# Performance work log

Hardware: AMD Instinct MI355X
Metric: run time of the kernel (lower is better)

The kernel has to match this reference:

```python
import jax, jax.numpy as jnp
import numpy as np

B, KEY, D, U, MODES = 16384, 64, 128, 128, 32

def setup_inputs() -> dict:
    key = jax.random.key(0)
    k1, k2, k3, k4, k5 = jax.random.split(key, 5)
    return {
        "key": jax.random.normal(k1, (B, KEY), dtype=jnp.float32),
        "x": jax.random.normal(k2, (B, D), dtype=jnp.float32),
        "sens": jnp.ones((MODES,), dtype=jnp.float32),
        "keys_map": jax.random.normal(k3, (MODES, KEY), dtype=jnp.float32),
        "kernels": jax.random.normal(k4, (MODES, D, U), dtype=jnp.float32) * 0.05,
        "biases": jax.random.normal(k5, (MODES, U), dtype=jnp.float32) * 0.05,
    }

def reference(key, x, sens, keys_map, kernels, biases):
    # key: [B, KEY]; keys_map: [MODES, KEY]
    # Euclidean distance of each key to each mode's stored key.
    dist = jnp.sqrt(jnp.sum((key[:, None, :] - keys_map[None, :, :]) ** 2, axis=-1))  # [B, MODES]
    sim = jax.nn.softmax(sens / (dist + 1.0), axis=-1)  # [B, MODES]
    modes = kernels.shape[0]
    # Original: kernel_b = mean_m(sim[b,m] * kernels[m]); out_b = x_b @ kernel_b.
    # Reordered as GEMM-per-mode + weighted combine (same math):
    out = jnp.einsum('bm,bd,mdu->bu', sim, x, kernels) / modes  # [B, U]
    out = out + (sim @ biases) / modes  # mean over modes of sim-weighted biases
    return out
```

## Files before the change

kernel.cpp:

```cpp
#include <hip/hip_runtime.h>

#define BATCH 16384
#define KEYD  64
#define DDIM  128
#define UDIM  128
#define MODES 32

typedef __attribute__((ext_vector_type(8))) short bf16x8;
typedef __attribute__((ext_vector_type(4))) float f32x4;

__device__ __forceinline__ unsigned short f2bf(float f) {
  unsigned u = __float_as_uint(f);
  unsigned r = (u + 0x7FFFu + ((u >> 16) & 1u)) >> 16;
  return (unsigned short)r;
}

__device__ __forceinline__ void gld_lds16(const void* g, void* l) {
  __builtin_amdgcn_global_load_lds(
      (const __attribute__((address_space(1))) unsigned int*)g,
      (__attribute__((address_space(3))) unsigned int*)l, 16, 0, 0);
}

__global__ __launch_bounds__(256) void prep_all(
    const float* __restrict__ key, const float* __restrict__ x,
    const float* __restrict__ sens, const float* __restrict__ keys_map,
    const float* __restrict__ kernels, const float* __restrict__ biases,
    float* __restrict__ sim, unsigned short* __restrict__ x16,
    unsigned short* __restrict__ kb16, unsigned short* __restrict__ bb16) {
  const int t = threadIdx.x;
  const int bid = blockIdx.x;

  if (bid < BATCH / 32) {
    __shared__ float kr[32][KEYD];
    *(float4*)(&kr[0][0] + t * 4) =
        *(const float4*)(key + (long)bid * 32 * KEYD + t * 4);
    *(float4*)(&kr[0][0] + 1024 + t * 4) =
        *(const float4*)(key + (long)bid * 32 * KEYD + 1024 + t * 4);

    const int lane = t & 63, wave = t >> 6;
    const int m = lane & 31, h = lane >> 5;
    float kreg[32];
    {
      const float* kmp = keys_map + m * KEYD + h * 32;
      #pragma unroll
      for (int j = 0; j < 32; j += 4) {
        const float4 v = *(const float4*)(kmp + j);
        kreg[j] = v.x; kreg[j + 1] = v.y; kreg[j + 2] = v.z; kreg[j + 3] = v.w;
      }
    }
    const float sv = sens[m];
    __syncthreads();

    #pragma unroll
    for (int rr = 0; rr < 8; ++rr) {
      const int rl = wave * 8 + rr;
      const long row = (long)bid * 32 + rl;

      float d2h = 0.f;
      #pragma unroll
      for (int j = 0; j < 32; j += 2) {
        const float2 kv = *(const float2*)(&kr[rl][h * 32 + j]);
        float a = kv.x - kreg[j], b = kv.y - kreg[j + 1];
        d2h += a * a + b * b;
      }
      float d2 = d2h + __shfl_xor(d2h, 32, 64);
      float logit = sv / (sqrtf(d2) + 1.0f);
      float mx = logit;
      #pragma unroll
      for (int off = 16; off > 0; off >>= 1) mx = fmaxf(mx, __shfl_xor(mx, off, 64));
      float e = __expf(logit - mx);
      float s = e;
      #pragma unroll
      for (int off = 16; off > 0; off >>= 1) s += __shfl_xor(s, off, 64);
      if (h == 0) sim[row * MODES + m] = e / s;

      const float2 xv = *(const float2*)(x + row * DDIM + lane * 2);
      ushort2 o; o.x = f2bf(xv.x); o.y = f2bf(xv.y);
      *(ushort2*)(x16 + row * DDIM + lane * 2) = o;
    }
  } else {
    int tt = (bid - BATCH / 32) * 256 + t;
    if (tt < MODES * 16 * UDIM) {
      int u = tt & 127, kb = (tt >> 7) & 15, m = tt >> 11;
      const float* src = kernels + (long)((m * 16 + kb) * 8) * UDIM + u;
      ushort4 lo, hi;
      lo.x = f2bf(src[0 * UDIM]); lo.y = f2bf(src[1 * UDIM]);
      lo.z = f2bf(src[2 * UDIM]); lo.w = f2bf(src[3 * UDIM]);
      hi.x = f2bf(src[4 * UDIM]); hi.y = f2bf(src[5 * UDIM]);
      hi.z = f2bf(src[6 * UDIM]); hi.w = f2bf(src[7 * UDIM]);
      *(ushort4*)(kb16 + (long)tt * 8) = lo;
      *(ushort4*)(kb16 + (long)tt * 8 + 4) = hi;
    } else {
      int tb = tt - MODES * 16 * UDIM;
      int u = tb & 127, kb = tb >> 7;
      const float* src = biases + kb * 8 * UDIM + u;
      ushort4 lo, hi;
      lo.x = f2bf(src[0 * UDIM]); lo.y = f2bf(src[1 * UDIM]);
      lo.z = f2bf(src[2 * UDIM]); lo.w = f2bf(src[3 * UDIM]);
      hi.x = f2bf(src[4 * UDIM]); hi.y = f2bf(src[5 * UDIM]);
      hi.z = f2bf(src[6 * UDIM]); hi.w = f2bf(src[7 * UDIM]);
      *(ushort4*)(bb16 + (long)tb * 8) = lo;
      *(ushort4*)(bb16 + (long)tb * 8 + 4) = hi;
    }
  }
}

#define MODE_STRIDE (16 * UDIM * 8)

__global__ __launch_bounds__(512, 2) void gemm_fused(
    const unsigned short* __restrict__ x16, const unsigned short* __restrict__ kb16,
    const unsigned short* __restrict__ bb16, const float* __restrict__ sim,
    float* __restrict__ out) {
  __shared__ alignas(16) unsigned short bsh[2][MODE_STRIDE];
  __shared__ float simT[MODES][64];

  const int t = threadIdx.x;
  const int lane = t & 63, w = t >> 6;
  const int q = lane >> 4, l16 = lane & 15;
  const long bm = (long)blockIdx.x * 64;
  const int ucol = w * 16 + l16;

  {
    const int r = t >> 3, mg = (t & 7) * 4;
    const float4 v = *(const float4*)(sim + (bm + r) * MODES + mg);
    simT[mg + 0][r] = v.x; simT[mg + 1][r] = v.y;
    simT[mg + 2][r] = v.z; simT[mg + 3][r] = v.w;
  }

  bf16x8 aF[4][4];
  #pragma unroll
  for (int rt = 0; rt < 4; ++rt)
    #pragma unroll
    for (int ks = 0; ks < 4; ++ks)
      aF[rt][ks] = *(const bf16x8*)(x16 + (bm + rt * 16 + l16) * DDIM + ks * 32 + q * 8);

  #pragma unroll
  for (int i = 0; i < 4; ++i) {
    const int off = (t + i * 512) * 8;
    gld_lds16(kb16 + off, &bsh[0][off]);
  }

  f32x4 acc[4] = {};

  for (int mi = 0; mi < MODES; ++mi) {
    __syncthreads();
    if (mi < MODES - 1) {
      const unsigned short* src = kb16 + (long)(mi + 1) * MODE_STRIDE;
      unsigned short* dst = bsh[(mi + 1) & 1];
      #pragma unroll
      for (int i = 0; i < 4; ++i) {
        const int off = (t + i * 512) * 8;
        gld_lds16(src + off, dst + off);
      }
    }

    const unsigned short* bs = bsh[mi & 1];
    bf16x8 bF[4];
    #pragma unroll
    for (int ks = 0; ks < 4; ++ks)
      bF[ks] = *(const bf16x8*)&bs[(((ks * 4 + q) * UDIM) + ucol) * 8];

    f32x4 tmp[4] = {};
    #pragma unroll
    for (int ks = 0; ks < 4; ++ks)
      #pragma unroll
      for (int rt = 0; rt < 4; ++rt)
        tmp[rt] = __builtin_amdgcn_mfma_f32_16x16x32_bf16(aF[rt][ks], bF[ks], tmp[rt], 0, 0, 0);

    #pragma unroll
    for (int rt = 0; rt < 4; ++rt) {
      const f32x4 s = *(const f32x4*)&simT[mi][rt * 16 + q * 4];
      acc[rt] += s * tmp[rt];
    }
  }

  {
    const bf16x8 bb = *(const bf16x8*)(bb16 + ((long)q * UDIM + ucol) * 8);
    #pragma unroll
    for (int rt = 0; rt < 4; ++rt) {
      const float* sp = sim + (bm + rt * 16 + l16) * MODES + q * 8;
      const float4 sv0 = *(const float4*)(sp);
      const float4 sv1 = *(const float4*)(sp + 4);
      bf16x8 sF;
      sF[0] = (short)f2bf(sv0.x); sF[1] = (short)f2bf(sv0.y);
      sF[2] = (short)f2bf(sv0.z); sF[3] = (short)f2bf(sv0.w);
      sF[4] = (short)f2bf(sv1.x); sF[5] = (short)f2bf(sv1.y);
      sF[6] = (short)f2bf(sv1.z); sF[7] = (short)f2bf(sv1.w);
      acc[rt] = __builtin_amdgcn_mfma_f32_16x16x32_bf16(sF, bb, acc[rt], 0, 0, 0);
    }
  }

  #pragma unroll
  for (int rt = 0; rt < 4; ++rt) {
    const long row = bm + rt * 16 + q * 4;
    #pragma unroll
    for (int r = 0; r < 4; ++r)
      out[(row + r) * UDIM + ucol] = acc[rt][r] * (1.0f / MODES);
  }
}

extern "C" void kernel_launch(void* const* d_in, const int* in_sizes, int n_in,
                              void* d_out, int out_size, void* d_ws, size_t ws_size,
                              hipStream_t stream) {
  const float* key      = (const float*)d_in[0];
  const float* x        = (const float*)d_in[1];
  const float* sens     = (const float*)d_in[2];
  const float* keys_map = (const float*)d_in[3];
  const float* kernels  = (const float*)d_in[4];
  const float* biases   = (const float*)d_in[5];
  float* out = (float*)d_out;

  char* ws = (char*)d_ws;
  float*          sim  = (float*)ws;
  unsigned short* x16  = (unsigned short*)(ws + (2u << 20));
  unsigned short* kb16 = (unsigned short*)(ws + (6u << 20));
  unsigned short* bb16 = (unsigned short*)(ws + (7u << 20));

  prep_all<<<BATCH / 32 + 258, 256, 0, stream>>>(
      key, x, sens, keys_map, kernels, biases, sim, x16, kb16, bb16);
  gemm_fused<<<dim3(BATCH / 64), 512, 0, stream>>>(x16, kb16, bb16, sim, out);
}
```

Measured before the change: 114.5 us.

## Split GEMM output columns across two blocks and process two modes per stage

```diff
diff --git a/kernel.cpp b/kernel.cpp
--- a/kernel.cpp
+++ b/kernel.cpp
@@ -106,25 +106,30 @@
 }
 
 #define MODE_STRIDE (16 * UDIM * 8)
-
-__global__ __launch_bounds__(512, 2) void gemm_fused(
+#define HALF_STRIDE (16 * 64 * 8)
+
+__global__ __launch_bounds__(256, 2) void gemm_fused(
     const unsigned short* __restrict__ x16, const unsigned short* __restrict__ kb16,
     const unsigned short* __restrict__ bb16, const float* __restrict__ sim,
     float* __restrict__ out) {
-  __shared__ alignas(16) unsigned short bsh[2][MODE_STRIDE];
+  __shared__ alignas(16) unsigned short bsh[2][2 * HALF_STRIDE];
   __shared__ float simT[MODES][64];
 
   const int t = threadIdx.x;
   const int lane = t & 63, w = t >> 6;
   const int q = lane >> 4, l16 = lane & 15;
   const long bm = (long)blockIdx.x * 64;
-  const int ucol = w * 16 + l16;
+  const int ch = blockIdx.y;
+  const int uc = w * 16 + l16;
 
   {
-    const int r = t >> 3, mg = (t & 7) * 4;
-    const float4 v = *(const float4*)(sim + (bm + r) * MODES + mg);
-    simT[mg + 0][r] = v.x; simT[mg + 1][r] = v.y;
-    simT[mg + 2][r] = v.z; simT[mg + 3][r] = v.w;
+    const int r = t >> 2, mg = (t & 3) * 8;
+    const float4 v0 = *(const float4*)(sim + (bm + r) * MODES + mg);
+    const float4 v1 = *(const float4*)(sim + (bm + r) * MODES + mg + 4);
+    simT[mg + 0][r] = v0.x; simT[mg + 1][r] = v0.y;
+    simT[mg + 2][r] = v0.z; simT[mg + 3][r] = v0.w;
+    simT[mg + 4][r] = v1.x; simT[mg + 5][r] = v1.y;
+    simT[mg + 6][r] = v1.z; simT[mg + 7][r] = v1.w;
   }
 
   bf16x8 aF[4][4];
@@ -135,47 +140,53 @@
       aF[rt][ks] = *(const bf16x8*)(x16 + (bm + rt * 16 + l16) * DDIM + ks * 32 + q * 8);
 
   #pragma unroll
-  for (int i = 0; i < 4; ++i) {
-    const int off = (t + i * 512) * 8;
-    gld_lds16(kb16 + off, &bsh[0][off]);
+  for (int i = 0; i < 8; ++i) {
+    const int c = i * 4 + w, ml = c >> 4, kb = c & 15;
+    gld_lds16(kb16 + (long)ml * MODE_STRIDE + kb * (UDIM * 8) + ch * (64 * 8) + lane * 8,
+              &bsh[0][(c * 64 + lane) * 8]);
   }
 
   f32x4 acc[4] = {};
 
-  for (int mi = 0; mi < MODES; ++mi) {
+  for (int s = 0; s < MODES / 2; ++s) {
     __syncthreads();
-    if (mi < MODES - 1) {
-      const unsigned short* src = kb16 + (long)(mi + 1) * MODE_STRIDE;
-      unsigned short* dst = bsh[(mi + 1) & 1];
-      #pragma unroll
-      for (int i = 0; i < 4; ++i) {
-        const int off = (t + i * 512) * 8;
-        gld_lds16(src + off, dst + off);
-      }
-    }
-
-    const unsigned short* bs = bsh[mi & 1];
-    bf16x8 bF[4];
-    #pragma unroll
-    for (int ks = 0; ks < 4; ++ks)
-      bF[ks] = *(const bf16x8*)&bs[(((ks * 4 + q) * UDIM) + ucol) * 8];
-
-    f32x4 tmp[4] = {};
-    #pragma unroll
-    for (int ks = 0; ks < 4; ++ks)
-      #pragma unroll
-      for (int rt = 0; rt < 4; ++rt)
-        tmp[rt] = __builtin_amdgcn_mfma_f32_16x16x32_bf16(aF[rt][ks], bF[ks], tmp[rt], 0, 0, 0);
-
-    #pragma unroll
-    for (int rt = 0; rt < 4; ++rt) {
-      const f32x4 s = *(const f32x4*)&simT[mi][rt * 16 + q * 4];
-      acc[rt] += s * tmp[rt];
+    if (s < MODES / 2 - 1) {
+      const unsigned short* srcb = kb16 + (long)(s + 1) * 2 * MODE_STRIDE;
+      unsigned short* dst = bsh[(s + 1) & 1];
+      #pragma unroll
+      for (int i = 0; i < 8; ++i) {
+        const int c = i * 4 + w, ml = c >> 4, kb = c & 15;
+        gld_lds16(srcb + (long)ml * MODE_STRIDE + kb * (UDIM * 8) + ch * (64 * 8) + lane * 8,
+                  dst + (c * 64 + lane) * 8);
+      }
+    }
+
+    const unsigned short* bs = bsh[s & 1];
+    #pragma unroll
+    for (int ml = 0; ml < 2; ++ml) {
+      const int mi = s * 2 + ml;
+      bf16x8 bF[4];
+      #pragma unroll
+      for (int ks = 0; ks < 4; ++ks)
+        bF[ks] = *(const bf16x8*)&bs[ml * HALF_STRIDE + (((ks * 4 + q) * 64) + uc) * 8];
+
+      f32x4 tmp[4] = {};
+      #pragma unroll
+      for (int ks = 0; ks < 4; ++ks)
+        #pragma unroll
+        for (int rt = 0; rt < 4; ++rt)
+          tmp[rt] = __builtin_amdgcn_mfma_f32_16x16x32_bf16(aF[rt][ks], bF[ks], tmp[rt], 0, 0, 0);
+
+      #pragma unroll
+      for (int rt = 0; rt < 4; ++rt) {
+        const f32x4 sv = *(const f32x4*)&simT[mi][rt * 16 + q * 4];
+        acc[rt] += sv * tmp[rt];
+      }
     }
   }
 
   {
-    const bf16x8 bb = *(const bf16x8*)(bb16 + ((long)q * UDIM + ucol) * 8);
+    const bf16x8 bb = *(const bf16x8*)(bb16 + ((long)q * UDIM + ch * 64 + uc) * 8);
     #pragma unroll
     for (int rt = 0; rt < 4; ++rt) {
       const float* sp = sim + (bm + rt * 16 + l16) * MODES + q * 8;
@@ -195,7 +206,7 @@
     const long row = bm + rt * 16 + q * 4;
     #pragma unroll
     for (int r = 0; r < 4; ++r)
-      out[(row + r) * UDIM + ucol] = acc[rt][r] * (1.0f / MODES);
+      out[(row + r) * UDIM + ch * 64 + uc] = acc[rt][r] * (1.0f / MODES);
   }
 }
 
@@ -218,5 +229,5 @@
 
   prep_all<<<BATCH / 32 + 258, 256, 0, stream>>>(
       key, x, sens, keys_map, kernels, biases, sim, x16, kb16, bb16);
-  gemm_fused<<<dim3(BATCH / 64), 512, 0, stream>>>(x16, kb16, bb16, sim, out);
-}
+  gemm_fused<<<dim3(BATCH / 64, 2), 256, 0, stream>>>(x16, kb16, bb16, sim, out);
+}
```

New measurement: 107.9 us. 1.06x faster.

## Restructure mode-weighted GEMM into U-strip blocks with per-strip kernel slices

Applied to the files above, without the earlier changes.

```diff
diff --git a/kernel.cpp b/kernel.cpp
--- a/kernel.cpp
+++ b/kernel.cpp
@@ -25,13 +25,15 @@
     const float* __restrict__ key, const float* __restrict__ x,
     const float* __restrict__ sens, const float* __restrict__ keys_map,
     const float* __restrict__ kernels, const float* __restrict__ biases,
-    float* __restrict__ sim, unsigned short* __restrict__ x16,
+    float* __restrict__ sim, float* __restrict__ simT,
+    unsigned short* __restrict__ x16,
     unsigned short* __restrict__ kb16, unsigned short* __restrict__ bb16) {
   const int t = threadIdx.x;
   const int bid = blockIdx.x;
 
   if (bid < BATCH / 32) {
     __shared__ float kr[32][KEYD];
+    __shared__ float sims[32][33];
     *(float4*)(&kr[0][0] + t * 4) =
         *(const float4*)(key + (long)bid * 32 * KEYD + t * 4);
     *(float4*)(&kr[0][0] + 1024 + t * 4) =
@@ -72,11 +74,24 @@
       float s = e;
       #pragma unroll
       for (int off = 16; off > 0; off >>= 1) s += __shfl_xor(s, off, 64);
-      if (h == 0) sim[row * MODES + m] = e / s;
+      if (h == 0) {
+        const float p = e / s;
+        sim[row * MODES + m] = p;
+        sims[m][rl] = p;
+      }
 
       const float2 xv = *(const float2*)(x + row * DDIM + lane * 2);
       ushort2 o; o.x = f2bf(xv.x); o.y = f2bf(xv.y);
       *(ushort2*)(x16 + row * DDIM + lane * 2) = o;
+    }
+
+    __syncthreads();
+    {
+      const int m2 = t >> 3, r0 = (t & 7) * 4;
+      float4 v;
+      v.x = sims[m2][r0 + 0]; v.y = sims[m2][r0 + 1];
+      v.z = sims[m2][r0 + 2]; v.w = sims[m2][r0 + 3];
+      *(float4*)(simT + (long)m2 * BATCH + (long)bid * 32 + r0) = v;
     }
   } else {
     int tt = (bid - BATCH / 32) * 256 + t;
@@ -105,80 +120,99 @@
   }
 }
 
-#define MODE_STRIDE (16 * UDIM * 8)
-
-__global__ __launch_bounds__(512, 2) void gemm_fused(
+__global__ __launch_bounds__(256, 1) void gemm_strip(
     const unsigned short* __restrict__ x16, const unsigned short* __restrict__ kb16,
     const unsigned short* __restrict__ bb16, const float* __restrict__ sim,
-    float* __restrict__ out) {
-  __shared__ alignas(16) unsigned short bsh[2][MODE_STRIDE];
-  __shared__ float simT[MODES][64];
+    const float* __restrict__ simT, float* __restrict__ out) {
+  __shared__ alignas(16) unsigned short bshB[256 * 16 * 8];
 
   const int t = threadIdx.x;
   const int lane = t & 63, w = t >> 6;
   const int q = lane >> 4, l16 = lane & 15;
-  const long bm = (long)blockIdx.x * 64;
-  const int ucol = w * 16 + l16;
+  const int bid = blockIdx.x;
+  const int group = bid & 31, strip = bid >> 5;
+  const long bm = (long)group * 512;
+  const int wrow = w * 128;
+
+  #pragma unroll
+  for (int i = 0; i < 16; ++i) {
+    const int j = i * 4 + w;
+    const int c = 4 * j + (lane >> 4);
+    const int m_l = c >> 4, kb = c & 15;
+    gld_lds16(kb16 + ((long)m_l * 16 + kb) * (UDIM * 8) + (strip * 16 + (lane & 15)) * 8,
+              &bshB[(c * 16 + (lane & 15)) * 8]);
+  }
+
+  bf16x8 aF[8][4];
+  #pragma unroll
+  for (int rt = 0; rt < 8; ++rt)
+    #pragma unroll
+    for (int ks = 0; ks < 4; ++ks)
+      aF[rt][ks] = *(const bf16x8*)(x16 + (bm + wrow + rt * 16 + l16) * DDIM + ks * 32 + q * 8);
+
+  __syncthreads();
+
+  bf16x8 pf[16];
+  #pragma unroll
+  for (int i = 0; i < 16; ++i) {
+    const int j = i * 4 + w;
+    const int c = 4 * j + (lane >> 4);
+    const int m_l = c >> 4, kb = c & 15;
+    pf[i] = *(const bf16x8*)(kb16 + ((long)(16 + m_l) * 16 + kb) * (UDIM * 8)
+                             + (strip * 16 + (lane & 15)) * 8);
+  }
+
+  f32x4 acc[8] = {};
+  const float* svbase = simT + bm + wrow + q * 4;
+
+#define LOAD_SV(dst, mg)                                                        \
+  { _Pragma("unroll")                                                           \
+    for (int rt = 0; rt < 8; ++rt)                                              \
+      dst[rt] = *(const f32x4*)(svbase + (long)(mg) * BATCH + rt * 16); }
+
+#define COMPUTE_MODE(ml, SV)                                                    \
+  { bf16x8 bF[4];                                                               \
+    _Pragma("unroll")                                                           \
+    for (int ks = 0; ks < 4; ++ks)                                              \
+      bF[ks] = *(const bf16x8*)&bshB[(((ml) * 16 + ks * 4 + q) * 16 + l16) * 8];\
+    _Pragma("unroll")                                                           \
+    for (int rt = 0; rt < 8; ++rt) {                                            \
+      f32x4 tmp = {};                                                           \
+      _Pragma("unroll")                                                         \
+      for (int ks = 0; ks < 4; ++ks)                                            \
+        tmp = __builtin_amdgcn_mfma_f32_16x16x32_bf16(aF[rt][ks], bF[ks], tmp, 0, 0, 0); \
+      acc[rt] += SV[rt] * tmp;                                                  \
+    } }
+
+  for (int h = 0; h < 2; ++h) {
+    if (h == 1) {
+      __syncthreads();
+      #pragma unroll
+      for (int i = 0; i < 16; ++i) {
+        const int j = i * 4 + w;
+        const int c = 4 * j + (lane >> 4);
+        *(bf16x8*)&bshB[(c * 16 + (lane & 15)) * 8] = pf[i];
+      }
+      __syncthreads();
+    }
+    f32x4 svA[8], svB[8];
+    LOAD_SV(svA, h * 16);
+    #pragma unroll 2
+    for (int ml = 0; ml < 16; ml += 2) {
+      LOAD_SV(svB, h * 16 + ml + 1);
+      COMPUTE_MODE(ml, svA);
+      if (ml + 2 < 16) LOAD_SV(svA, h * 16 + ml + 2);
+      COMPUTE_MODE(ml + 1, svB);
+    }
+  }
+#undef LOAD_SV
+#undef COMPUTE_MODE
 
   {
-    const int r = t >> 3, mg = (t & 7) * 4;
-    const float4 v = *(const float4*)(sim + (bm + r) * MODES + mg);
-    simT[mg + 0][r] = v.x; simT[mg + 1][r] = v.y;
-    simT[mg + 2][r] = v.z; simT[mg + 3][r] = v.w;
-  }
-
-  bf16x8 aF[4][4];
-  #pragma unroll
-  for (int rt = 0; rt < 4; ++rt)
-    #pragma unroll
-    for (int ks = 0; ks < 4; ++ks)
-      aF[rt][ks] = *(const bf16x8*)(x16 + (bm + rt * 16 + l16) * DDIM + ks * 32 + q * 8);
-
-  #pragma unroll
-  for (int i = 0; i < 4; ++i) {
-    const int off = (t + i * 512) * 8;
-    gld_lds16(kb16 + off, &bsh[0][off]);
-  }
-
-  f32x4 acc[4] = {};
-
-  for (int mi = 0; mi < MODES; ++mi) {
-    __syncthreads();
-    if (mi < MODES - 1) {
-      const unsigned short* src = kb16 + (long)(mi + 1) * MODE_STRIDE;
-      unsigned short* dst = bsh[(mi + 1) & 1];
-      #pragma unroll
-      for (int i = 0; i < 4; ++i) {
-        const int off = (t + i * 512) * 8;
-        gld_lds16(src + off, dst + off);
-      }
-    }
-
-    const unsigned short* bs = bsh[mi & 1];
-    bf16x8 bF[4];
-    #pragma unroll
-    for (int ks = 0; ks < 4; ++ks)
-      bF[ks] = *(const bf16x8*)&bs[(((ks * 4 + q) * UDIM) + ucol) * 8];
-
-    f32x4 tmp[4] = {};
-    #pragma unroll
-    for (int ks = 0; ks < 4; ++ks)
-      #pragma unroll
-      for (int rt = 0; rt < 4; ++rt)
-        tmp[rt] = __builtin_amdgcn_mfma_f32_16x16x32_bf16(aF[rt][ks], bF[ks], tmp[rt], 0, 0, 0);
-
-    #pragma unroll
-    for (int rt = 0; rt < 4; ++rt) {
-      const f32x4 s = *(const f32x4*)&simT[mi][rt * 16 + q * 4];
-      acc[rt] += s * tmp[rt];
-    }
-  }
-
-  {
-    const bf16x8 bb = *(const bf16x8*)(bb16 + ((long)q * UDIM + ucol) * 8);
-    #pragma unroll
-    for (int rt = 0; rt < 4; ++rt) {
-      const float* sp = sim + (bm + rt * 16 + l16) * MODES + q * 8;
+    const bf16x8 bb = *(const bf16x8*)(bb16 + ((long)q * UDIM + strip * 16 + l16) * 8);
+    #pragma unroll
+    for (int rt = 0; rt < 8; ++rt) {
+      const float* sp = sim + (bm + wrow + rt * 16 + l16) * MODES + q * 8;
       const float4 sv0 = *(const float4*)(sp);
       const float4 sv1 = *(const float4*)(sp + 4);
       bf16x8 sF;
@@ -191,11 +225,11 @@
   }
 
   #pragma unroll
-  for (int rt = 0; rt < 4; ++rt) {
-    const long row = bm + rt * 16 + q * 4;
+  for (int rt = 0; rt < 8; ++rt) {
+    const long row = bm + wrow + rt * 16 + q * 4;
     #pragma unroll
     for (int r = 0; r < 4; ++r)
-      out[(row + r) * UDIM + ucol] = acc[rt][r] * (1.0f / MODES);
+      out[(row + r) * UDIM + strip * 16 + l16] = acc[rt][r] * (1.0f / MODES);
   }
 }
 
@@ -215,8 +249,9 @@
   unsigned short* x16  = (unsigned short*)(ws + (2u << 20));
   unsigned short* kb16 = (unsigned short*)(ws + (6u << 20));
   unsigned short* bb16 = (unsigned short*)(ws + (7u << 20));
+  float*          simT = (float*)(ws + (8u << 20));
 
   prep_all<<<BATCH / 32 + 258, 256, 0, stream>>>(
-      key, x, sens, keys_map, kernels, biases, sim, x16, kb16, bb16);
-  gemm_fused<<<dim3(BATCH / 64), 512, 0, stream>>>(x16, kb16, bb16, sim, out);
-}
+      key, x, sens, keys_map, kernels, biases, sim, simT, x16, kb16, bb16);
+  gemm_strip<<<dim3(256), 256, 0, stream>>>(x16, kb16, bb16, sim, simT, out);
+}
```

New measurement: 106.6 us. -6.9%, faster.
